# Kernel optimization log

Hardware: AMD Instinct MI355X
Metric: run time of the kernel (lower is better)

The kernel has to match this reference:

```python
import jax, jax.numpy as jnp
import numpy as np

L, B, I, H = 256, 16, 2048, 2048
S = R = T = 32  # s_size == t_size is required by the read-hop chaining


def setup_inputs() -> dict:
    key = jax.random.key(0)
    ks = jax.random.split(key, 8)
    def p(k, shape, scale=0.02):
        return jax.random.normal(k, shape, jnp.float32) * scale
    return dict(
        inputs=jax.random.normal(ks[0], (L, B, I), jnp.float32),
        h0=jnp.zeros((B, H), jnp.float32),
        c0=jnp.zeros((B, H), jnp.float32),
        F0=jnp.zeros((B, S * R, T), jnp.float32),
        W_ih=p(ks[1], (4 * H, I)),
        W_hh=p(ks[2], (4 * H, H)),
        b_ih=jnp.zeros((4 * H,), jnp.float32),
        b_hh=jnp.zeros((4 * H,), jnp.float32),
        Ww_w=p(ks[3], (S + R + T + 1, H)),
        Ww_b=jnp.zeros((S + R + T + 1,), jnp.float32),
        Wr_w=p(ks[4], (S + 3 * R, H)),
        Wr_b=jnp.zeros((S + 3 * R,), jnp.float32),
        Wlin_w=p(ks[5], (H, T)),
        Wlin_b=jnp.zeros((H,), jnp.float32),
    )


def _ln(x, eps=1e-5):
    # LayerNorm without affine params (elementwise_affine=False)
    m = jnp.mean(x, -1, keepdims=True)
    v = jnp.var(x, -1, keepdims=True)
    return (x - m) * jax.lax.rsqrt(v + eps)


def reference(inputs, h0, c0, F0, W_ih, W_hh, b_ih, b_hh,
              Ww_w, Ww_b, Wr_w, Wr_b, Wlin_w, Wlin_b):
    # ---- single-layer LSTM (PyTorch gate order i,f,g,o) ----
    bias = b_ih + b_hh
    def lstm_step(carry, x_t):
        h, c = carry
        g = x_t @ W_ih.T + h @ W_hh.T + bias            # [B,4H]
        i, f, gg, o = jnp.split(g, 4, axis=-1)
        c = jax.nn.sigmoid(f) * c + jax.nn.sigmoid(i) * jnp.tanh(gg)
        h = jax.nn.sigmoid(o) * jnp.tanh(c)
        return (h, c), h
    _, x = jax.lax.scan(lstm_step, (h0, c0), inputs)     # x: [L,B,H]

    # ---- Fast Weight Memory: per-step write then 3-hop read ----
    def fwm_step(Fm, x_t):
        # write
        w = x_t @ Ww_w.T + Ww_b                          # [B, S+R+T+1]
        s = jnp.tanh(w[:, :S])
        r = jnp.tanh(w[:, S:S + R])
        t = jnp.tanh(w[:, S + R:S + R + T])
        b = jax.nn.sigmoid(w[:, S + R + T:] + 1.0)       # [B,1]
        sr = (s[:, :, None] * r[:, None, :]).reshape(-1, S * R)   # [B,S*R]
        v = jnp.einsum('bk,bkt->bt', sr, Fm)             # [B,T]
        Fm = Fm + sr[:, :, None] * (b * (t - v))[:, None, :]
        n = jnp.linalg.norm(Fm.reshape(Fm.shape[0], -1), axis=-1)
        Fm = Fm / (jax.nn.relu(n - 1.0) + 1.0)[:, None, None]
        # read (3 hops)
        rv = jnp.tanh(x_t @ Wr_w.T + Wr_b)               # [B, S+3R]
        q = rv[:, :S]
        for j in range(3):
            rj = rv[:, S + j * R:S + (j + 1) * R]
            nr = (q[:, :, None] * rj[:, None, :]).reshape(q.shape[0], -1)
            q = _ln(jnp.einsum('bk,bkt->bt', nr, Fm))    # [B,T]
        return Fm, q

    _, qs = jax.lax.scan(fwm_step, F0, x)                # qs: [L,B,T]
    return x + qs @ Wlin_w.T + Wlin_b                    # [L,B,H]
```

## Files before the change

### kernel.cpp

```cpp
#include <hip/hip_runtime.h>
#include <hip/hip_bf16.h>
#include <cstdint>
#include <cstddef>

#define L_DIM 256
#define B_DIM 16
#define I_DIM 2048
#define H_DIM 2048
#define G4    8192
#define MROWS 4096
#define NWGL  128
#define NPRJ  16
#define NSCN  16

typedef __hip_bfloat16 bf16;
typedef __bf16 bf16x8_t __attribute__((ext_vector_type(8)));
typedef _Float16 f16x8_t __attribute__((ext_vector_type(8)));
typedef _Float16 f16x4_t __attribute__((ext_vector_type(4)));
typedef float f32x4_t   __attribute__((ext_vector_type(4)));

__device__ __forceinline__ bf16 f2b(float f) { return __float2bfloat16(f); }

__device__ __forceinline__ void gl_lds16(const void* g, void* l) {
  __builtin_amdgcn_global_load_lds(
      (const __attribute__((address_space(1))) unsigned int*)g,
      (__attribute__((address_space(3))) unsigned int*)l, 16, 0, 0);
}

__device__ __forceinline__ float sigmoidf_(float x) { return 1.f / (1.f + expf(-x)); }

__device__ __forceinline__ f16x8_t load_f16x8_sc(const _Float16* p) {
  f16x8_t r;
  asm volatile("global_load_dwordx4 %0, %1, off sc0 sc1" : "=v"(r) : "v"(p));
  return r;
}
__device__ __forceinline__ bf16x8_t load_bf16x8_sc(const bf16* p) {
  bf16x8_t r;
  asm volatile("global_load_dwordx4 %0, %1, off sc0 sc1" : "=v"(r) : "v"(p));
  return r;
}
__device__ __forceinline__ float load_f32_sc(const float* p) {
  float r;
  asm volatile("global_load_dword %0, %1, off sc0 sc1" : "=v"(r) : "v"(p));
  return r;
}
__device__ __forceinline__ unsigned int load_u16_sc(const _Float16* p) {
  unsigned int r;
  asm volatile("global_load_ushort %0, %1, off sc0 sc1" : "=v"(r) : "v"(p));
  return r;
}
__device__ __forceinline__ void store_short_sc(void* p, unsigned int v) {
  asm volatile("global_store_short %0, %1, off sc0 sc1" :: "v"(p), "v"(v) : "memory");
}
__device__ __forceinline__ void store_f32_sc(void* p, float v) {
  asm volatile("global_store_dword %0, %1, off sc0 sc1" :: "v"(p), "v"(v) : "memory");
}

__global__ void prep_kernel(const float* __restrict__ Wih, const float* __restrict__ Whh,
                            const float* __restrict__ inp, const float* __restrict__ Www,
                            const float* __restrict__ Wwb, const float* __restrict__ Wrw,
                            const float* __restrict__ h0,
                            _Float16* __restrict__ Wih_f, _Float16* __restrict__ Whh_f,
                            _Float16* __restrict__ inp_f,
                            bf16* __restrict__ Wq_hi, bf16* __restrict__ Wq_lo,
                            bf16* __restrict__ Wr_hi, bf16* __restrict__ Wr_lo,
                            float* __restrict__ wbpad,
                            _Float16* __restrict__ Xh0)
{
  size_t idx0 = (size_t)blockIdx.x * blockDim.x + threadIdx.x;
  size_t stride = (size_t)gridDim.x * blockDim.x;
  for (size_t i = idx0; i < 16777216ull; i += stride) {
    Wih_f[i] = (_Float16)Wih[i];
    Whh_f[i] = (_Float16)Whh[i];
  }
  for (size_t i = idx0; i < 8388608ull; i += stride) inp_f[i] = (_Float16)inp[i];
  for (size_t i = idx0; i < 262144ull; i += stride) {
    size_t r = i >> 11;
    float q = (r < 97) ? Www[i] : 0.f;
    bf16 qh = f2b(q);
    Wq_hi[i] = qh;
    Wq_lo[i] = f2b(q - (float)qh);
    float rr = Wrw[i];
    bf16 rh = f2b(rr);
    Wr_hi[i] = rh;
    Wr_lo[i] = f2b(rr - (float)rh);
  }
  for (size_t i = idx0; i < 128ull; i += stride) wbpad[i] = (i < 97) ? Wwb[i] : 0.f;
  for (size_t i = idx0; i < 32768ull; i += stride) Xh0[i] = (_Float16)h0[i];
}

__global__ __launch_bounds__(256) void gemm_f16(const _Float16* __restrict__ A,
                                                const _Float16* __restrict__ B,
                                                const float* __restrict__ bih,
                                                const float* __restrict__ bhh,
                                                _Float16* __restrict__ Gin2,
                                                int M, int N, int K)
{
  __shared__ __align__(16) _Float16 As[128 * 32];
  __shared__ __align__(16) _Float16 Bs[128 * 32];
  const int tid  = threadIdx.x;
  const int lane = tid & 63;
  const int w    = tid >> 6;
  const int wm   = w >> 1, wn = w & 1;
  const int m0   = blockIdx.x * 128, n0 = blockIdx.y * 128;

  f32x4_t acc[4][4];
#pragma unroll
  for (int m = 0; m < 4; ++m)
#pragma unroll
    for (int n = 0; n < 4; ++n) acc[m][n] = (f32x4_t){0.f, 0.f, 0.f, 0.f};

  for (int k0 = 0; k0 < K; k0 += 32) {
#pragma unroll
    for (int r = 0; r < 2; ++r) {
      const int base = w * 2048 + r * 1024;
      const int off  = base + lane * 16;
      const int e    = off >> 1;
      const int row  = e >> 5;
      const int col  = e & 31;
      gl_lds16(A + (size_t)(m0 + row) * K + (k0 + col), (char*)As + base);
      gl_lds16(B + (size_t)(n0 + row) * K + (k0 + col), (char*)Bs + base);
    }
    __syncthreads();

    f16x8_t af[4], bfr[4];
    const int kb = (lane >> 4) * 16;
#pragma unroll
    for (int m = 0; m < 4; ++m)
      af[m] = *reinterpret_cast<const f16x8_t*>((const char*)As + (wm * 64 + m * 16 + (lane & 15)) * 64 + kb);
#pragma unroll
    for (int n = 0; n < 4; ++n)
      bfr[n] = *reinterpret_cast<const f16x8_t*>((const char*)Bs + (wn * 64 + n * 16 + (lane & 15)) * 64 + kb);
#pragma unroll
    for (int m = 0; m < 4; ++m)
#pragma unroll
      for (int n = 0; n < 4; ++n)
        acc[m][n] = __builtin_amdgcn_mfma_f32_16x16x32_f16(af[m], bfr[n], acc[m][n], 0, 0, 0);
    __syncthreads();
  }

  const int jj = lane & 15;
#pragma unroll
  for (int n = 0; n < 4; ++n) {
    const int colb = n0 + wn * 64 + n * 16;
    const int gate = colb >> 11;
    const int wg   = (colb & 2047) >> 4;
    const float bv = bih[colb + jj] + bhh[colb + jj];
#pragma unroll
    for (int m = 0; m < 4; ++m) {
      const int rowb = m0 + wm * 64 + m * 16;
      const int t = rowb >> 4;
      f16x4_t v4;
#pragma unroll
      for (int r = 0; r < 4; ++r) v4[r] = (_Float16)(acc[m][n][r] + bv);
      *reinterpret_cast<f16x4_t*>(
          Gin2 + (((size_t)t * NWGL + wg) * 4 + gate) * 256 + jj * 16 + (lane >> 4) * 4) = v4;
    }
  }
}

__global__ __launch_bounds__(512, 2) void fused_rnn(
    const _Float16* __restrict__ Whh,
    const _Float16* __restrict__ Gin2,
    const float* __restrict__ bih, const float* __restrict__ bhh,
    const float* __restrict__ c0,
    const bf16* __restrict__ Wq_hi, const bf16* __restrict__ Wq_lo,
    const bf16* __restrict__ Wr_hi, const bf16* __restrict__ Wr_lo,
    const float* __restrict__ wbpad, const float* __restrict__ Wrb,
    const float* __restrict__ F0,
    _Float16* __restrict__ Xh,
    bf16* __restrict__ XhHi, bf16* __restrict__ XhLo,
    float* __restrict__ Wall, float* __restrict__ RVall,
    _Float16* __restrict__ Gbuf,
    int* lflags, int* pflags)
{
  __shared__ float part[8][4][16][17];
  __shared__ float s_s[32], s_r[32], s_tv[32], s_bb;
  __shared__ float s_rv[128];
  __shared__ float s_v[32];
  __shared__ float s_red[8];

  const int wgid = blockIdx.x;
  const int tid  = threadIdx.x;
  const int lane = tid & 63;
  const int wv   = tid >> 6;

  if (wgid < NWGL) {
    const int wg = wgid;
    const int j0 = wg * 16;
    const int kw = wv * 256;

    f16x8_t whh[4][8];
    {
      const int nn  = lane & 15;
      const int kfo = (lane >> 4) * 8;
#pragma unroll
      for (int g = 0; g < 4; ++g) {
        const size_t grow = (size_t)(g * H_DIM + j0 + nn) * 2048;
#pragma unroll
        for (int ks = 0; ks < 8; ++ks)
          whh[g][ks] = *reinterpret_cast<const f16x8_t*>(Whh + grow + kw + ks * 32 + kfo);
      }
    }

    float c_reg = 0.f, cbr0 = 0.f, cbr1 = 0.f, cbr2 = 0.f, cbr3 = 0.f;
    if (tid < 256) {
      const int bb = tid & 15, jj = tid >> 4;
      const int j = j0 + jj;
      c_reg = c0[bb * H_DIM + j];
      cbr0 = bih[0 * H_DIM + j] + bhh[0 * H_DIM + j];
      cbr1 = bih[1 * H_DIM + j] + bhh[1 * H_DIM + j];
      cbr2 = bih[2 * H_DIM + j] + bhh[2 * H_DIM + j];
      cbr3 = bih[3 * H_DIM + j] + bhh[3 * H_DIM + j];
    }

    const size_t arow = (size_t)(lane & 15) * 2048 + kw + (lane >> 4) * 8;
    const int fidx = ((wv << 4) + (lane & 15)) << 4;

    for (int t = 0; t < L_DIM; ++t) {
      if (t > 0) {
        while (true) {
          const int v = __hip_atomic_load(&lflags[fidx], __ATOMIC_RELAXED,
                                          __HIP_MEMORY_SCOPE_AGENT);
          if (__all(v >= t)) break;
          __builtin_amdgcn_s_sleep(1);
        }
      }

      float gin0 = 0.f, gin1 = 0.f, gin2v = 0.f, gin3 = 0.f;
      if (tid < 256) {
        const _Float16* gbase = Gin2 + ((size_t)t * NWGL + wg) * 1024;
        gin0  = (float)gbase[0 * 256 + tid];
        gin1  = (float)gbase[1 * 256 + tid];
        gin2v = (float)gbase[2 * 256 + tid];
        gin3  = (float)gbase[3 * 256 + tid];
      }

      const size_t hoff = (size_t)t * 32768 + arow;
      f16x8_t hf[8];
#pragma unroll
      for (int ks = 0; ks < 8; ++ks)
        hf[ks] = load_f16x8_sc(Xh + hoff + ks * 32);
      asm volatile("s_waitcnt vmcnt(0)" ::: "memory");
      __builtin_amdgcn_sched_barrier(0);

      f32x4_t acc[4];
#pragma unroll
      for (int g = 0; g < 4; ++g) acc[g] = (f32x4_t){0.f, 0.f, 0.f, 0.f};
#pragma unroll
      for (int ks = 0; ks < 8; ++ks) {
#pragma unroll
        for (int g = 0; g < 4; ++g)
          acc[g] = __builtin_amdgcn_mfma_f32_16x16x32_f16(hf[ks], whh[g][ks], acc[g], 0, 0, 0);
      }
#pragma unroll
      for (int g = 0; g < 4; ++g)
#pragma unroll
        for (int r = 0; r < 4; ++r)
          part[wv][g][(lane >> 4) * 4 + r][lane & 15] = acc[g][r];
      __syncthreads();

      if (tid < 256) {
        const int bb = tid & 15, jj = tid >> 4;
        float g4[4] = {gin0, gin1, gin2v, gin3};
        const float cb4[4] = {cbr0, cbr1, cbr2, cbr3};
#pragma unroll
        for (int g = 0; g < 4; ++g) {
          float s = 0.f;
#pragma unroll
          for (int v = 0; v < 8; ++v) s += part[v][g][bb][jj];
          g4[g] += s + cb4[g];
        }
        const float i_ = sigmoidf_(g4[0]);
        const float f_ = sigmoidf_(g4[1]);
        const float g_ = tanhf(g4[2]);
        const float o_ = sigmoidf_(g4[3]);
        c_reg = f_ * c_reg + i_ * g_;
        const float h = o_ * tanhf(c_reg);
        const int bj = bb * 2048 + j0 + jj;
        const _Float16 hF = (_Float16)h;
        const bf16 hhv = f2b(h);
        const bf16 hlv = f2b(h - (float)hhv);
        const size_t xi = ((size_t)t * 16 + bb) * 2048 + j0 + jj;
        store_short_sc(Xh + (size_t)(t + 1) * 32768 + bj,
                       (unsigned int)__builtin_bit_cast(unsigned short, hF));
        store_short_sc(XhHi + xi,
                       (unsigned int)__builtin_bit_cast(unsigned short, hhv));
        store_short_sc(XhLo + xi,
                       (unsigned int)__builtin_bit_cast(unsigned short, hlv));
      }
      asm volatile("s_waitcnt vmcnt(0)" ::: "memory");
      __syncthreads();

      if (tid == 0)
        __hip_atomic_store(&lflags[wg << 4], t + 1, __ATOMIC_RELAXED,
                           __HIP_MEMORY_SCOPE_AGENT);
    }

  } else if (wgid < NWGL + NPRJ) {
    const int p   = wgid - NWGL;
    const int kw  = wv * 256;
    const int nn  = lane & 15;
    const int kfo = (lane >> 4) * 8;

    bf16x8_t wbh[8], wbl[8];
    {
      const bf16* Bh = (p < 8) ? Wq_hi : Wr_hi;
      const bf16* Bl = (p < 8) ? Wq_lo : Wr_lo;
      const int brow = (p < 8) ? (p * 16 + nn) : ((p - 8) * 16 + nn);
#pragma unroll
      for (int ks = 0; ks < 8; ++ks) {
        const size_t o = (size_t)brow * 2048 + kw + ks * 32 + kfo;
        wbh[ks] = *reinterpret_cast<const bf16x8_t*>(Bh + o);
        wbl[ks] = *reinterpret_cast<const bf16x8_t*>(Bl + o);
      }
    }
    float biasv = 0.f;
    if (tid < 256) {
      const int oo = tid >> 4;
      biasv = (p < 8) ? wbpad[p * 16 + oo] : Wrb[(p - 8) * 16 + oo];
    }

    const size_t axrow = (size_t)(lane & 15) * 2048 + kw + kfo;

    for (int t = 0; t < L_DIM; ++t) {
      while (true) {
        const int v0 = __hip_atomic_load(&lflags[lane << 4], __ATOMIC_RELAXED,
                                         __HIP_MEMORY_SCOPE_AGENT);
        const int v1 = __hip_atomic_load(&lflags[(64 + lane) << 4], __ATOMIC_RELAXED,
                                         __HIP_MEMORY_SCOPE_AGENT);
        if (__all(v0 > t && v1 > t)) break;
        __builtin_amdgcn_s_sleep(1);
      }

      const size_t xoff = (size_t)t * 32768 + axrow;
      bf16x8_t xh[8], xl[8];
#pragma unroll
      for (int ks = 0; ks < 8; ++ks) {
        xh[ks] = load_bf16x8_sc(XhHi + xoff + ks * 32);
        xl[ks] = load_bf16x8_sc(XhLo + xoff + ks * 32);
      }
      asm volatile("s_waitcnt vmcnt(0)" ::: "memory");
      __builtin_amdgcn_sched_barrier(0);

      f32x4_t acc = {0.f, 0.f, 0.f, 0.f};
#pragma unroll
      for (int ks = 0; ks < 8; ++ks) {
        acc = __builtin_amdgcn_mfma_f32_16x16x32_bf16(xh[ks], wbh[ks], acc, 0, 0, 0);
        acc = __builtin_amdgcn_mfma_f32_16x16x32_bf16(xh[ks], wbl[ks], acc, 0, 0, 0);
        acc = __builtin_amdgcn_mfma_f32_16x16x32_bf16(xl[ks], wbh[ks], acc, 0, 0, 0);
      }
#pragma unroll
      for (int r = 0; r < 4; ++r)
        part[wv][0][(lane >> 4) * 4 + r][lane & 15] = acc[r];
      __syncthreads();

      if (tid < 256) {
        const int bb = tid & 15, oo = tid >> 4;
        float s = 0.f;
#pragma unroll
        for (int v = 0; v < 8; ++v) s += part[v][0][bb][oo];
        s += biasv;
        float* dst;
        if (p < 8) {
          dst = Wall + (size_t)(t * 16 + bb) * 128 + p * 16 + oo;
        } else {
          s = tanhf(s);
          dst = RVall + (size_t)(t * 16 + bb) * 128 + (p - 8) * 16 + oo;
        }
        store_f32_sc(dst, s);
      }
      asm volatile("s_waitcnt vmcnt(0)" ::: "memory");
      __syncthreads();

      if (tid == 0)
        __hip_atomic_store(&pflags[p << 4], t + 1, __ATOMIC_RELAXED,
                           __HIP_MEMORY_SCOPE_AGENT);
    }

  } else {
    const int b     = wgid - NWGL - NPRJ;
    const int si    = lane >> 1;
    const int rbase = 16 * (lane & 1);
    const int tl    = lane & 31;

    float F[16][4];
#pragma unroll
    for (int i = 0; i < 16; ++i)
#pragma unroll
      for (int j = 0; j < 4; ++j)
        F[i][j] = F0[((size_t)b * 1024 + (16 * lane + i)) * 32 + 4 * wv + j];

    float N = 0.f;
    {
      float loc = 0.f;
#pragma unroll
      for (int i = 0; i < 16; ++i)
#pragma unroll
        for (int j = 0; j < 4; ++j) loc += F[i][j] * F[i][j];
#pragma unroll
      for (int m = 1; m < 64; m <<= 1) loc += __shfl_xor(loc, m);
      if (lane == 0) s_red[wv] = loc;
      __syncthreads();
#pragma unroll
      for (int k = 0; k < 8; ++k) N += s_red[k];
    }

    for (int t = 0; t < 256; ++t) {
      while (true) {
        const int v = __hip_atomic_load(&pflags[(lane & 15) << 4], __ATOMIC_RELAXED,
                                        __HIP_MEMORY_SCOPE_AGENT);
        if (__all(v > t)) break;
        __builtin_amdgcn_s_sleep(1);
      }

      float wpre = 0.f, rvpre = 0.f;
      if (tid < 97)  wpre = load_f32_sc(Wall + (size_t)(t * 16 + b) * 128 + tid);
      if (tid >= 128 && tid < 256)
        rvpre = load_f32_sc(RVall + (size_t)(t * 16 + b) * 128 + tid - 128);
      asm volatile("s_waitcnt vmcnt(0)" ::: "memory");
      __syncthreads();
      if (tid < 32)       s_s[tid]       = tanhf(wpre);
      else if (tid < 64)  s_r[tid - 32]  = tanhf(wpre);
      else if (tid < 96)  s_tv[tid - 64] = tanhf(wpre);
      else if (tid == 96) s_bb           = sigmoidf_(wpre + 1.f);
      else if (tid >= 128 && tid < 256) s_rv[tid - 128] = rvpre;
      __syncthreads();

      const float sv = s_s[si];
      float sr[16];
#pragma unroll
      for (int i = 0; i < 16; ++i) sr[i] = sv * s_r[rbase + i];

      float vv4[4];
#pragma unroll
      for (int j = 0; j < 4; ++j) {
        float pp = 0.f;
#pragma unroll
        for (int i = 0; i < 16; ++i) pp += sr[i] * F[i][j];
#pragma unroll
        for (int m = 1; m < 64; m <<= 1) pp += __shfl_xor(pp, m);
        vv4[j] = pp;
      }
      if (lane == 0) {
#pragma unroll
        for (int j = 0; j < 4; ++j) s_v[4 * wv + j] = vv4[j];
      }
      __syncthreads();

      const float vt  = s_v[tl];
      const float ut  = s_bb * (s_tv[tl] - vt);
      const float sl  = s_s[tl];
      const float rl  = s_r[tl];
      float uv = ut * vt, uu = ut * ut, ss = sl * sl, rr = rl * rl;
#pragma unroll
      for (int m = 1; m < 32; m <<= 1) {
        uv += __shfl_xor(uv, m);
        uu += __shfl_xor(uu, m);
        ss += __shfl_xor(ss, m);
        rr += __shfl_xor(rr, m);
      }
      const float Np  = N + 2.f * uv + ss * rr * uu;
      const float n_  = sqrtf(Np);
      const float inv = 1.f / (fmaxf(n_ - 1.f, 0.f) + 1.f);
      N = Np * inv * inv;

      float uw[4];
#pragma unroll
      for (int j = 0; j < 4; ++j) uw[j] = __shfl(ut, 4 * wv + j);
#pragma unroll
      for (int i = 0; i < 16; ++i)
#pragma unroll
        for (int j = 0; j < 4; ++j)
          F[i][j] = (F[i][j] + sr[i] * uw[j]) * inv;

      _Float16* gout = Gbuf + ((size_t)(t * 16 + b) * 3) * 1024;
#pragma unroll
      for (int jit = 0; jit < 3; ++jit) {
        float rjv[16];
#pragma unroll
        for (int i = 0; i < 16; ++i) rjv[i] = s_rv[32 + 32 * jit + rbase + i];
        f16x4_t gv;
#pragma unroll
        for (int j = 0; j < 4; ++j) {
          float g = 0.f;
#pragma unroll
          for (int i = 0; i < 16; ++i) g += rjv[i] * F[i][j];
          g += __shfl_xor(g, 1);
          gv[j] = (_Float16)g;
        }
        if ((lane & 1) == 0)
          *reinterpret_cast<f16x4_t*>(gout + jit * 1024 + (lane >> 1) * 32 + 4 * wv) = gv;
      }
    }
  }
}

__global__ __launch_bounds__(256) void qread_out(const _Float16* __restrict__ Gbuf,
                                                 const float* __restrict__ RVall,
                                                 const bf16* __restrict__ Xh1Hi,
                                                 const bf16* __restrict__ Xh1Lo,
                                                 const float* __restrict__ Wlin,
                                                 const float* __restrict__ blin,
                                                 float* __restrict__ out)
{
  __shared__ float qs[32];
  const int row = blockIdx.x;
  const int tid = threadIdx.x;

  if (tid < 64) {
    const int lane  = tid;
    const int tq    = lane & 31;
    const int ihalf = (lane >> 5) * 16;
    const _Float16* G = Gbuf + (size_t)row * 3 * 1024;
    float q = RVall[(size_t)row * 128 + tq];
#pragma unroll 1
    for (int jit = 0; jit < 3; ++jit) {
      float c = 0.f;
#pragma unroll
      for (int i = 0; i < 16; ++i) {
        const float qi = __shfl(q, ihalf + i);
        c += qi * (float)G[jit * 1024 + (ihalf + i) * 32 + tq];
      }
      c += __shfl_xor(c, 32);
      float mval = c;
#pragma unroll
      for (int m = 1; m < 32; m <<= 1) mval += __shfl_xor(mval, m);
      mval *= (1.f / 32.f);
      const float dl = c - mval;
      float var = dl * dl;
#pragma unroll
      for (int m = 1; m < 32; m <<= 1) var += __shfl_xor(var, m);
      var *= (1.f / 32.f);
      q = dl * rsqrtf(var + 1e-5f);
    }
    if (lane < 32) qs[lane] = q;
  }
  __syncthreads();

  for (int h = tid; h < H_DIM; h += 256) {
    const size_t xi = (size_t)row * H_DIM + h;
    float acc = (float)Xh1Hi[xi] + (float)Xh1Lo[xi] + blin[h];
    const float* wr = Wlin + (size_t)h * 32;
#pragma unroll
    for (int t2 = 0; t2 < 32; ++t2) acc += qs[t2] * wr[t2];
    out[xi] = acc;
  }
}

extern "C" void kernel_launch(void* const* d_in, const int* in_sizes, int n_in,
                              void* d_out, int out_size, void* d_ws, size_t ws_size,
                              hipStream_t stream)
{
  (void)in_sizes; (void)n_in; (void)out_size; (void)ws_size;
  const float* inp  = (const float*)d_in[0];
  const float* h0   = (const float*)d_in[1];
  const float* c0   = (const float*)d_in[2];
  const float* F0   = (const float*)d_in[3];
  const float* Wih  = (const float*)d_in[4];
  const float* Whh  = (const float*)d_in[5];
  const float* bih  = (const float*)d_in[6];
  const float* bhh  = (const float*)d_in[7];
  const float* Www  = (const float*)d_in[8];
  const float* Wwb  = (const float*)d_in[9];
  const float* Wrw  = (const float*)d_in[10];
  const float* Wrb  = (const float*)d_in[11];
  const float* Wlin = (const float*)d_in[12];
  const float* blin = (const float*)d_in[13];
  float* out = (float*)d_out;

  char* p = (char*)d_ws;
  auto alloc = [&](size_t bytes) {
    char* r = p;
    p += (bytes + 255) & ~(size_t)255;
    return r;
  };
  _Float16* Whh_f = (_Float16*)alloc(16777216ull * 2);
  _Float16* Wih_f = (_Float16*)alloc(16777216ull * 2);
  _Float16* inp_f = (_Float16*)alloc(8388608ull * 2);
  _Float16* Gin2  = (_Float16*)alloc(33554432ull * 2);
  _Float16* Xh    = (_Float16*)alloc(257ull * 32768 * 2);
  bf16*     XhLo  = (bf16*)alloc(8388608ull * 2);
  bf16*  Wq_hi  = (bf16*)alloc(262144ull * 2);
  bf16*  Wq_lo  = (bf16*)alloc(262144ull * 2);
  bf16*  Wr_hi  = (bf16*)alloc(262144ull * 2);
  bf16*  Wr_lo  = (bf16*)alloc(262144ull * 2);
  float* wbpad  = (float*)alloc(128ull * 4);
  float* Wall   = (float*)alloc(524288ull * 4);
  float* RVall  = (float*)alloc(524288ull * 4);
  _Float16* Gbuf = (_Float16*)alloc(12582912ull * 2);
  int*   flags  = (int*)alloc((NWGL + NPRJ) * 64);
  int*   lflags = flags;
  int*   pflags = flags + NWGL * 16;
  bf16*  XhHi  = (bf16*)inp_f;

  prep_kernel<<<2048, 256, 0, stream>>>(Wih, Whh, inp, Www, Wwb, Wrw, h0,
                                        Wih_f, Whh_f, inp_f,
                                        Wq_hi, Wq_lo, Wr_hi, Wr_lo, wbpad, Xh);

  gemm_f16<<<dim3(32, 64), 256, 0, stream>>>(inp_f, Wih_f, bih, bhh, Gin2,
                                             MROWS, G4, 2048);

  hipMemsetAsync(flags, 0, (NWGL + NPRJ) * 64, stream);
  {
    void* kargs[] = {
      (void*)&Whh_f, (void*)&Gin2, (void*)&bih, (void*)&bhh, (void*)&c0,
      (void*)&Wq_hi, (void*)&Wq_lo, (void*)&Wr_hi, (void*)&Wr_lo,
      (void*)&wbpad, (void*)&Wrb, (void*)&F0,
      (void*)&Xh, (void*)&XhHi, (void*)&XhLo,
      (void*)&Wall, (void*)&RVall, (void*)&Gbuf,
      (void*)&lflags, (void*)&pflags
    };
    hipLaunchCooperativeKernel((const void*)fused_rnn,
                               dim3(NWGL + NPRJ + NSCN), dim3(512),
                               kargs, 0, stream);
  }

  qread_out<<<4096, 256, 0, stream>>>(Gbuf, RVall, XhHi, XhLo, Wlin, blin, out);
}
```

Before: 1.873 ms.

## Replace flag-based inter-workgroup sync with sentinel-value polling on data buffers

Removes the per-step atomic flag stores and flag polling between the LSTM, projection and scan workgroups. Instead, the prep kernel fills the hidden-state, hi/lo split and projection buffers with NaN-like sentinel patterns, and consumers spin-reload the data until no sentinel remains. This drops the store-drain wait and the flag round trip from each recurrence step, shortening the critical path. In exchange it adds sentinel-fill writes in prep, a dedicated XhHi buffer instead of aliasing inp_f, and a correctness risk if a real value ever equals a sentinel bit pattern.

```diff
diff --git a/kernel.cpp b/kernel.cpp
--- a/kernel.cpp
+++ b/kernel.cpp
@@ -13,11 +13,16 @@
 #define NPRJ  16
 #define NSCN  16
 
+#define SENT_F16  0x7C01u
+#define SENT_BF16 0x7FC1u
+#define SENT_F32  0x7FC00000u
+
 typedef __hip_bfloat16 bf16;
 typedef __bf16 bf16x8_t __attribute__((ext_vector_type(8)));
 typedef _Float16 f16x8_t __attribute__((ext_vector_type(8)));
 typedef _Float16 f16x4_t __attribute__((ext_vector_type(4)));
 typedef float f32x4_t   __attribute__((ext_vector_type(4)));
+typedef unsigned int u32x4 __attribute__((ext_vector_type(4)));
 
 __device__ __forceinline__ bf16 f2b(float f) { return __float2bfloat16(f); }
 
@@ -44,16 +49,32 @@
   asm volatile("global_load_dword %0, %1, off sc0 sc1" : "=v"(r) : "v"(p));
   return r;
 }
-__device__ __forceinline__ unsigned int load_u16_sc(const _Float16* p) {
-  unsigned int r;
-  asm volatile("global_load_ushort %0, %1, off sc0 sc1" : "=v"(r) : "v"(p));
-  return r;
-}
 __device__ __forceinline__ void store_short_sc(void* p, unsigned int v) {
   asm volatile("global_store_short %0, %1, off sc0 sc1" :: "v"(p), "v"(v) : "memory");
 }
 __device__ __forceinline__ void store_f32_sc(void* p, float v) {
   asm volatile("global_store_dword %0, %1, off sc0 sc1" :: "v"(p), "v"(v) : "memory");
+}
+
+__device__ __forceinline__ unsigned sent16x8(f16x8_t v, unsigned pat) {
+  const u32x4 u = __builtin_bit_cast(u32x4, v);
+  unsigned b = 0;
+#pragma unroll
+  for (int i = 0; i < 4; ++i) {
+    b |= ((u[i] & 0xFFFFu) == pat);
+    b |= ((u[i] >> 16) == pat);
+  }
+  return b;
+}
+__device__ __forceinline__ unsigned sentb16x8(bf16x8_t v, unsigned pat) {
+  const u32x4 u = __builtin_bit_cast(u32x4, v);
+  unsigned b = 0;
+#pragma unroll
+  for (int i = 0; i < 4; ++i) {
+    b |= ((u[i] & 0xFFFFu) == pat);
+    b |= ((u[i] >> 16) == pat);
+  }
+  return b;
 }
 
 __global__ void prep_kernel(const float* __restrict__ Wih, const float* __restrict__ Whh,
@@ -65,7 +86,9 @@
                             bf16* __restrict__ Wq_hi, bf16* __restrict__ Wq_lo,
                             bf16* __restrict__ Wr_hi, bf16* __restrict__ Wr_lo,
                             float* __restrict__ wbpad,
-                            _Float16* __restrict__ Xh0)
+                            _Float16* __restrict__ Xh,
+                            bf16* __restrict__ XhHi, bf16* __restrict__ XhLo,
+                            float* __restrict__ Wall, float* __restrict__ RVall)
 {
   size_t idx0 = (size_t)blockIdx.x * blockDim.x + threadIdx.x;
   size_t stride = (size_t)gridDim.x * blockDim.x;
@@ -73,7 +96,16 @@
     Wih_f[i] = (_Float16)Wih[i];
     Whh_f[i] = (_Float16)Whh[i];
   }
-  for (size_t i = idx0; i < 8388608ull; i += stride) inp_f[i] = (_Float16)inp[i];
+  for (size_t i = idx0; i < 8388608ull; i += stride) {
+    inp_f[i] = (_Float16)inp[i];
+    ((unsigned short*)Xh)[32768 + i]   = (unsigned short)SENT_F16;
+    ((unsigned short*)XhHi)[i]         = (unsigned short)SENT_BF16;
+    ((unsigned short*)XhLo)[i]         = (unsigned short)SENT_BF16;
+  }
+  for (size_t i = idx0; i < 524288ull; i += stride) {
+    ((unsigned int*)Wall)[i]  = SENT_F32;
+    ((unsigned int*)RVall)[i] = SENT_F32;
+  }
   for (size_t i = idx0; i < 262144ull; i += stride) {
     size_t r = i >> 11;
     float q = (r < 97) ? Www[i] : 0.f;
@@ -86,7 +118,7 @@
     Wr_lo[i] = f2b(rr - (float)rh);
   }
   for (size_t i = idx0; i < 128ull; i += stride) wbpad[i] = (i < 97) ? Wwb[i] : 0.f;
-  for (size_t i = idx0; i < 32768ull; i += stride) Xh0[i] = (_Float16)h0[i];
+  for (size_t i = idx0; i < 32768ull; i += stride) Xh[i] = (_Float16)h0[i];
 }
 
 __global__ __launch_bounds__(256) void gemm_f16(const _Float16* __restrict__ A,
@@ -171,8 +203,7 @@
     _Float16* __restrict__ Xh,
     bf16* __restrict__ XhHi, bf16* __restrict__ XhLo,
     float* __restrict__ Wall, float* __restrict__ RVall,
-    _Float16* __restrict__ Gbuf,
-    int* lflags, int* pflags)
+    _Float16* __restrict__ Gbuf)
 {
   __shared__ float part[8][4][16][17];
   __shared__ float s_s[32], s_r[32], s_tv[32], s_bb;
@@ -215,18 +246,8 @@
     }
 
     const size_t arow = (size_t)(lane & 15) * 2048 + kw + (lane >> 4) * 8;
-    const int fidx = ((wv << 4) + (lane & 15)) << 4;
 
     for (int t = 0; t < L_DIM; ++t) {
-      if (t > 0) {
-        while (true) {
-          const int v = __hip_atomic_load(&lflags[fidx], __ATOMIC_RELAXED,
-                                          __HIP_MEMORY_SCOPE_AGENT);
-          if (__all(v >= t)) break;
-          __builtin_amdgcn_s_sleep(1);
-        }
-      }
-
       float gin0 = 0.f, gin1 = 0.f, gin2v = 0.f, gin3 = 0.f;
       if (tid < 256) {
         const _Float16* gbase = Gin2 + ((size_t)t * NWGL + wg) * 1024;
@@ -238,10 +259,18 @@
 
       const size_t hoff = (size_t)t * 32768 + arow;
       f16x8_t hf[8];
-#pragma unroll
-      for (int ks = 0; ks < 8; ++ks)
-        hf[ks] = load_f16x8_sc(Xh + hoff + ks * 32);
-      asm volatile("s_waitcnt vmcnt(0)" ::: "memory");
+      while (true) {
+#pragma unroll
+        for (int ks = 0; ks < 8; ++ks)
+          hf[ks] = load_f16x8_sc(Xh + hoff + ks * 32);
+        asm volatile("s_waitcnt vmcnt(0)" ::: "memory");
+        __builtin_amdgcn_sched_barrier(0);
+        unsigned bad = 0;
+#pragma unroll
+        for (int ks = 0; ks < 8; ++ks) bad |= sent16x8(hf[ks], SENT_F16);
+        if (!__any(bad)) break;
+        __builtin_amdgcn_s_sleep(1);
+      }
       __builtin_amdgcn_sched_barrier(0);
 
       f32x4_t acc[4];
@@ -289,12 +318,7 @@
         store_short_sc(XhLo + xi,
                        (unsigned int)__builtin_bit_cast(unsigned short, hlv));
       }
-      asm volatile("s_waitcnt vmcnt(0)" ::: "memory");
-      __syncthreads();
-
-      if (tid == 0)
-        __hip_atomic_store(&lflags[wg << 4], t + 1, __ATOMIC_RELAXED,
-                           __HIP_MEMORY_SCOPE_AGENT);
+      __syncthreads();
     }
 
   } else if (wgid < NWGL + NPRJ) {
@@ -324,23 +348,25 @@
     const size_t axrow = (size_t)(lane & 15) * 2048 + kw + kfo;
 
     for (int t = 0; t < L_DIM; ++t) {
-      while (true) {
-        const int v0 = __hip_atomic_load(&lflags[lane << 4], __ATOMIC_RELAXED,
-                                         __HIP_MEMORY_SCOPE_AGENT);
-        const int v1 = __hip_atomic_load(&lflags[(64 + lane) << 4], __ATOMIC_RELAXED,
-                                         __HIP_MEMORY_SCOPE_AGENT);
-        if (__all(v0 > t && v1 > t)) break;
-        __builtin_amdgcn_s_sleep(1);
-      }
-
       const size_t xoff = (size_t)t * 32768 + axrow;
       bf16x8_t xh[8], xl[8];
-#pragma unroll
-      for (int ks = 0; ks < 8; ++ks) {
-        xh[ks] = load_bf16x8_sc(XhHi + xoff + ks * 32);
-        xl[ks] = load_bf16x8_sc(XhLo + xoff + ks * 32);
-      }
-      asm volatile("s_waitcnt vmcnt(0)" ::: "memory");
+      while (true) {
+#pragma unroll
+        for (int ks = 0; ks < 8; ++ks) {
+          xh[ks] = load_bf16x8_sc(XhHi + xoff + ks * 32);
+          xl[ks] = load_bf16x8_sc(XhLo + xoff + ks * 32);
+        }
+        asm volatile("s_waitcnt vmcnt(0)" ::: "memory");
+        __builtin_amdgcn_sched_barrier(0);
+        unsigned bad = 0;
+#pragma unroll
+        for (int ks = 0; ks < 8; ++ks) {
+          bad |= sentb16x8(xh[ks], SENT_BF16);
+          bad |= sentb16x8(xl[ks], SENT_BF16);
+        }
+        if (!__any(bad)) break;
+        __builtin_amdgcn_s_sleep(1);
+      }
       __builtin_amdgcn_sched_barrier(0);
 
       f32x4_t acc = {0.f, 0.f, 0.f, 0.f};
@@ -370,12 +396,7 @@
         }
         store_f32_sc(dst, s);
       }
-      asm volatile("s_waitcnt vmcnt(0)" ::: "memory");
-      __syncthreads();
-
-      if (tid == 0)
-        __hip_atomic_store(&pflags[p << 4], t + 1, __ATOMIC_RELAXED,
-                           __HIP_MEMORY_SCOPE_AGENT);
+      __syncthreads();
     }
 
   } else {
@@ -407,18 +428,21 @@
     }
 
     for (int t = 0; t < 256; ++t) {
-      while (true) {
-        const int v = __hip_atomic_load(&pflags[(lane & 15) << 4], __ATOMIC_RELAXED,
-                                        __HIP_MEMORY_SCOPE_AGENT);
-        if (__all(v > t)) break;
-        __builtin_amdgcn_s_sleep(1);
-      }
-
       float wpre = 0.f, rvpre = 0.f;
-      if (tid < 97)  wpre = load_f32_sc(Wall + (size_t)(t * 16 + b) * 128 + tid);
-      if (tid >= 128 && tid < 256)
-        rvpre = load_f32_sc(RVall + (size_t)(t * 16 + b) * 128 + tid - 128);
-      asm volatile("s_waitcnt vmcnt(0)" ::: "memory");
+      if (tid < 97) {
+        do {
+          wpre = load_f32_sc(Wall + (size_t)(t * 16 + b) * 128 + tid);
+          asm volatile("s_waitcnt vmcnt(0)" ::: "memory");
+          __builtin_amdgcn_sched_barrier(0);
+        } while (__builtin_bit_cast(unsigned int, wpre) == SENT_F32);
+      }
+      if (tid >= 128 && tid < 256) {
+        do {
+          rvpre = load_f32_sc(RVall + (size_t)(t * 16 + b) * 128 + tid - 128);
+          asm volatile("s_waitcnt vmcnt(0)" ::: "memory");
+          __builtin_amdgcn_sched_barrier(0);
+        } while (__builtin_bit_cast(unsigned int, rvpre) == SENT_F32);
+      }
       __syncthreads();
       if (tid < 32)       s_s[tid]       = tanhf(wpre);
       else if (tid < 64)  s_r[tid - 32]  = tanhf(wpre);
@@ -580,6 +604,7 @@
   _Float16* inp_f = (_Float16*)alloc(8388608ull * 2);
   _Float16* Gin2  = (_Float16*)alloc(33554432ull * 2);
   _Float16* Xh    = (_Float16*)alloc(257ull * 32768 * 2);
+  bf16*     XhHi  = (bf16*)alloc(8388608ull * 2);
   bf16*     XhLo  = (bf16*)alloc(8388608ull * 2);
   bf16*  Wq_hi  = (bf16*)alloc(262144ull * 2);
   bf16*  Wq_lo  = (bf16*)alloc(262144ull * 2);
@@ -589,27 +614,22 @@
   float* Wall   = (float*)alloc(524288ull * 4);
   float* RVall  = (float*)alloc(524288ull * 4);
   _Float16* Gbuf = (_Float16*)alloc(12582912ull * 2);
-  int*   flags  = (int*)alloc((NWGL + NPRJ) * 64);
-  int*   lflags = flags;
-  int*   pflags = flags + NWGL * 16;
-  bf16*  XhHi  = (bf16*)inp_f;
 
   prep_kernel<<<2048, 256, 0, stream>>>(Wih, Whh, inp, Www, Wwb, Wrw, h0,
                                         Wih_f, Whh_f, inp_f,
-                                        Wq_hi, Wq_lo, Wr_hi, Wr_lo, wbpad, Xh);
+                                        Wq_hi, Wq_lo, Wr_hi, Wr_lo, wbpad,
+                                        Xh, XhHi, XhLo, Wall, RVall);
 
   gemm_f16<<<dim3(32, 64), 256, 0, stream>>>(inp_f, Wih_f, bih, bhh, Gin2,
                                              MROWS, G4, 2048);
 
-  hipMemsetAsync(flags, 0, (NWGL + NPRJ) * 64, stream);
   {
     void* kargs[] = {
       (void*)&Whh_f, (void*)&Gin2, (void*)&bih, (void*)&bhh, (void*)&c0,
       (void*)&Wq_hi, (void*)&Wq_lo, (void*)&Wr_hi, (void*)&Wr_lo,
       (void*)&wbpad, (void*)&Wrb, (void*)&F0,
       (void*)&Xh, (void*)&XhHi, (void*)&XhLo,
-      (void*)&Wall, (void*)&RVall, (void*)&Gbuf,
-      (void*)&lflags, (void*)&pflags
+      (void*)&Wall, (void*)&RVall, (void*)&Gbuf
     };
     hipLaunchCooperativeKernel((const void*)fused_rnn,
                                dim3(NWGL + NPRJ + NSCN), dim3(512),
```

Result: slower. 2.026 ms (+8.1%).
